# Kernel tuning notes

Measured on AMD Instinct MI355X. Metric: run time of the kernel, lower is better.

## Reference

```python
import jax, jax.numpy as jnp
import numpy as np

HID = 128
MAX_NODES = 100000
MAX_EDGES = 300000
EVT_LEN = 4096
NUM_NODE = 20000
NUM_EDGE = 320000
# EVENT_TYPE_ID_MAP: pad=0 start=1 end=2 node-add=3 node-delete=4 edge-add=5 edge-delete=6
NODE_ADD, NODE_DEL = 3, 4


def time_encode(t, time_w, time_b):
    # TimeEncoder: cos(Linear(1 -> hidden)(t))
    return jnp.cos(t[..., None] * time_w + time_b)


def gru_cell(x, h, w_ih, w_hh, b_ih, b_hh):
    gi = x @ w_ih.T + b_ih
    gh = h @ w_hh.T + b_hh
    i_r, i_z, i_n = jnp.split(gi, 3, axis=-1)
    h_r, h_z, h_n = jnp.split(gh, 3, axis=-1)
    r = jax.nn.sigmoid(i_r + h_r)
    z = jax.nn.sigmoid(i_z + h_z)
    n = jnp.tanh(i_n + r * h_n)
    return (1.0 - z) * n + z * h


def setup_inputs() -> dict:
    key = jax.random.key(0)
    ks = jax.random.split(key, 32)
    H = HID
    s = 0.05
    inp = {}
    inp["event_type_ids"] = jax.random.randint(ks[0], (EVT_LEN,), 0, 7)
    inp["src_ids"] = jax.random.randint(ks[1], (EVT_LEN,), 0, MAX_NODES)
    inp["src_mask"] = (jax.random.uniform(ks[2], (EVT_LEN,)) > 0.3).astype(jnp.float32)
    inp["dst_ids"] = jax.random.randint(ks[3], (EVT_LEN,), 0, MAX_NODES)
    inp["dst_mask"] = (jax.random.uniform(ks[4], (EVT_LEN,)) > 0.3).astype(jnp.float32)
    inp["event_edge_ids"] = jax.random.randint(ks[5], (EVT_LEN,), 0, MAX_EDGES)
    inp["event_embeddings"] = jax.random.normal(ks[6], (EVT_LEN, H), dtype=jnp.float32)
    inp["event_mask"] = (jax.random.uniform(ks[7], (EVT_LEN,)) > 0.2).astype(jnp.float32)
    inp["event_timestamps"] = jax.random.uniform(ks[8], (EVT_LEN,)) * 100.0
    inp["node_ids"] = jax.random.randint(ks[9], (NUM_NODE,), 0, MAX_NODES)
    inp["edge_ids"] = jax.random.randint(ks[10], (NUM_EDGE,), 0, MAX_EDGES)
    inp["edge_index"] = jax.random.randint(ks[11], (2, NUM_EDGE), 0, NUM_NODE)
    inp["time"] = 100
    # persistent-buffer state
    inp["memory"] = jax.random.normal(ks[12], (MAX_NODES, H), dtype=jnp.float32) * s
    inp["last_update"] = jax.random.uniform(ks[13], (MAX_EDGES,)) * 50.0
    inp["node_features"] = jax.random.normal(ks[14], (MAX_NODES, H), dtype=jnp.float32) * s
    inp["edge_features"] = jax.random.normal(ks[15], (MAX_EDGES, H), dtype=jnp.float32) * s
    # TimeEncoder params (Linear(1, H))
    inp["time_w"] = jax.random.normal(ks[16], (H,), dtype=jnp.float32) * s
    inp["time_b"] = jax.random.normal(ks[17], (H,), dtype=jnp.float32) * s
    # GRUCell(5H -> H)
    inp["gru_w_ih"] = jax.random.normal(ks[18], (3 * H, 5 * H), dtype=jnp.float32) * s
    inp["gru_w_hh"] = jax.random.normal(ks[19], (3 * H, H), dtype=jnp.float32) * s
    inp["gru_b_ih"] = jax.random.normal(ks[20], (3 * H,), dtype=jnp.float32) * s
    inp["gru_b_hh"] = jax.random.normal(ks[21], (3 * H,), dtype=jnp.float32) * s
    # TransformerConv(H, H, heads=1, edge_dim=2H)
    inp["wq"] = jax.random.normal(ks[22], (H, H), dtype=jnp.float32) * s
    inp["bq"] = jax.random.normal(ks[23], (H,), dtype=jnp.float32) * s
    inp["wk"] = jax.random.normal(ks[24], (H, H), dtype=jnp.float32) * s
    inp["bk"] = jax.random.normal(ks[25], (H,), dtype=jnp.float32) * s
    inp["wv"] = jax.random.normal(ks[26], (H, H), dtype=jnp.float32) * s
    inp["bv"] = jax.random.normal(ks[27], (H,), dtype=jnp.float32) * s
    inp["we"] = jax.random.normal(ks[28], (H, 2 * H), dtype=jnp.float32) * s  # lin_edge, no bias
    inp["wskip"] = jax.random.normal(ks[29], (H, H), dtype=jnp.float32) * s
    inp["bskip"] = jax.random.normal(ks[30], (H,), dtype=jnp.float32) * s
    return inp


def reference(event_type_ids, src_ids, src_mask, dst_ids, dst_mask, event_edge_ids,
              event_embeddings, event_mask, event_timestamps, node_ids, edge_ids,
              edge_index, time, memory, last_update, node_features, edge_features,
              time_w, time_b, gru_w_ih, gru_w_hh, gru_b_ih, gru_b_hh,
              wq, bq, wk, bk, wv, bv, we, wskip, bskip):
    H = HID
    # ---- message() ----
    L = event_type_ids.shape[0]
    type_embs = jnp.broadcast_to(event_type_ids[:, None].astype(memory.dtype), (L, H))
    src_embs = memory[src_ids] * src_mask[:, None]
    dst_embs = memory[dst_ids] * dst_mask[:, None]
    edge_last = last_update[event_edge_ids]
    rel_ts = event_timestamps - edge_last * dst_mask
    is_node_ev = ((event_type_ids == NODE_ADD) | (event_type_ids == NODE_DEL)).astype(event_timestamps.dtype)
    ts_emb = time_encode(event_timestamps * is_node_ev + rel_ts * dst_mask, time_w, time_b) * event_mask[:, None]
    src_msgs = jnp.concatenate([type_embs, src_embs, dst_embs, ts_emb, event_embeddings], axis=1) * event_mask[:, None]
    dst_msgs = jnp.concatenate([type_embs, dst_embs, src_embs, ts_emb, event_embeddings], axis=1) * dst_mask[:, None]
    # ---- agg_message(): scatter-mean over node ids ----
    def agg(msgs, ids):
        s = jax.ops.segment_sum(msgs, ids, num_segments=MAX_NODES)
        c = jax.ops.segment_sum(jnp.ones((msgs.shape[0],), msgs.dtype), ids, num_segments=MAX_NODES)
        return s / jnp.maximum(c, 1.0)[:, None]
    agg_src = agg(src_msgs, src_ids)
    agg_dst = agg(dst_msgs, dst_ids)
    # ---- GRU memory update on unique ids ----
    # torch: memory[cat(uniq_src, uniq_dst)] = rnn(...); reads use pre-update memory,
    # dst writes come after src writes so they override on overlap. Duplicate ids in
    # src_ids carry identical per-id values, so scatter-set is equivalent to unique().
    new_src = gru_cell(agg_src[src_ids], memory[src_ids], gru_w_ih, gru_w_hh, gru_b_ih, gru_b_hh)
    new_dst = gru_cell(agg_dst[dst_ids], memory[dst_ids], gru_w_ih, gru_w_hh, gru_b_ih, gru_b_hh)
    memory = memory.at[src_ids].set(new_src)
    memory = memory.at[dst_ids].set(new_dst)
    # ---- edge attributes ----
    rel_t = time - last_update[edge_ids]
    rel_t_embs = time_encode(rel_t, time_w, time_b)
    edge_attr = jnp.concatenate([rel_t_embs, edge_features[edge_ids]], axis=-1)  # (E, 2H)
    # ---- TransformerConv (heads=1, concat, root_weight) ----
    x = node_features[node_ids] + memory[node_ids]  # (N, H)
    src, dst = edge_index[0], edge_index[1]
    q = x @ wq.T + bq
    k = x @ wk.T + bk
    v = x @ wv.T + bv
    e = edge_attr @ we.T  # lin_edge (no bias)
    alpha = jnp.sum(q[dst] * (k[src] + e), axis=-1) / jnp.sqrt(jnp.asarray(H, x.dtype))
    amax = jax.ops.segment_max(alpha, dst, num_segments=x.shape[0])
    ex = jnp.exp(alpha - amax[dst])
    denom = jax.ops.segment_sum(ex, dst, num_segments=x.shape[0])
    p = ex / jnp.maximum(denom[dst], 1e-16)
    out = jax.ops.segment_sum(p[:, None] * (v[src] + e), dst, num_segments=x.shape[0])
    return out + x @ wskip.T + bskip
```

## Files before the change

kernel.cpp:

```cpp
#include <hip/hip_runtime.h>
#include <math.h>

#define HID   128
#define MAXN  100000
#define MAXE  300000
#define EVT   4096
#define NNODE 20000
#define NEDGE 320000

typedef unsigned short u16;
typedef __attribute__((ext_vector_type(8))) short bf16x8;
typedef __attribute__((ext_vector_type(4))) float f32x4;

#define OFF_WIHB      0u
#define OFF_WHHB      491520u
#define OFF_WEB       589824u
#define OFF_WALLB     655360u
#define OFF_BALL      851968u
#define BASE2         855040u
#define OFF_REP_SRC   (BASE2 + 0u)
#define OFF_REP_DST   (BASE2 + 400128u)
#define OFF_CNT_SRC   (BASE2 + 800256u)
#define OFF_CNT_DST   (BASE2 + 1200384u)
#define OFF_SUM_SRC   (BASE2 + 1600512u)
#define OFF_SUM_DST   (BASE2 + 12086272u)
#define OFF_XGB       (BASE2 + 22572032u)
#define OFF_HG        (BASE2 + 33057792u)
#define OFF_HGB       (BASE2 + 37252096u)
#define OFF_GI        (BASE2 + 39349248u)
#define OFF_GH        (BASE2 + 51932160u)
#define OFF_NEWMEM    (BASE2 + 64515072u)
#define OFF_XB        (BASE2 + 0u)
#define OFF_QKVSE     (BASE2 + 5120000u)
#define OFF_KVB       (BASE2 + 66560000u)
#define OFF_DEG       (BASE2 + 76800000u)
#define OFF_OFFS      (BASE2 + 76880128u)
#define OFF_CURSOR    (BASE2 + 76960256u)
#define OFF_BSUM      (BASE2 + 77040384u)
#define OFF_SORTED    (BASE2 + 77041664u)
#define OFF_SACCB     (BASE2 + 78321664u)

__device__ __forceinline__ float sigmoidf_(float x) { return 1.f / (1.f + __expf(-x)); }
__device__ __forceinline__ u16 f2b(float f) {
    unsigned u = __float_as_uint(f);
    unsigned r = (u + 0x7fffu + ((u >> 16) & 1u)) >> 16;
    return (u16)r;
}
__device__ __forceinline__ float b2f(unsigned h) { return __uint_as_float(h << 16); }

__global__ void k_cvt(const float* __restrict__ s, u16* __restrict__ d, int n) {
    int i = blockIdx.x * blockDim.x + threadIdx.x;
    if (i < n) d[i] = f2b(s[i]);
}

__global__ void k_tables(const int* __restrict__ src_ids, const int* __restrict__ dst_ids,
                         unsigned* rep_src, unsigned* rep_dst, int* cnt_src, int* cnt_dst) {
    int i = blockIdx.x * blockDim.x + threadIdx.x;
    if (i >= EVT) return;
    int s = src_ids[i], d = dst_ids[i];
    atomicMin(&rep_src[s], (unsigned)i);
    atomicAdd(&cnt_src[s], 1);
    atomicMin(&rep_dst[d], (unsigned)i);
    atomicAdd(&cnt_dst[d], 1);
}

__global__ void k_message(const int* __restrict__ et_ids, const int* __restrict__ src_ids,
                          const float* __restrict__ src_mask, const int* __restrict__ dst_ids,
                          const float* __restrict__ dst_mask, const int* __restrict__ ev_eids,
                          const float* __restrict__ ev_emb, const float* __restrict__ ev_mask,
                          const float* __restrict__ ev_ts, const float* __restrict__ memory,
                          const float* __restrict__ last_update, const float* __restrict__ time_w,
                          const float* __restrict__ time_b, const unsigned* __restrict__ rep_src,
                          const unsigned* __restrict__ rep_dst, const int* __restrict__ cnt_src,
                          const int* __restrict__ cnt_dst, float* sum_src, float* sum_dst) {
    int i = blockIdx.x;
    int c = threadIdx.x;
    int et = et_ids[i];
    float sm = src_mask[i], dm = dst_mask[i], em = ev_mask[i], ts = ev_ts[i];
    int sid = src_ids[i], did = dst_ids[i], eid = ev_eids[i];
    float isnode = (et == 3 || et == 4) ? 1.f : 0.f;
    float rel = ts - last_update[eid] * dm;
    float tval = ts * isnode + rel * dm;
    float tse = __cosf(tval * time_w[c] + time_b[c]) * em;
    float typ = (float)et;
    float sv = memory[(size_t)sid * HID + c] * sm;
    float dv = memory[(size_t)did * HID + c] * dm;
    float ev = ev_emb[(size_t)i * HID + c];
    float* ps = sum_src + (size_t)rep_src[sid] * 640;
    if (cnt_src[sid] == 1) {
        ps[c] = typ * em; ps[128 + c] = sv * em; ps[256 + c] = dv * em;
        ps[384 + c] = tse * em; ps[512 + c] = ev * em;
    } else {
        atomicAdd(ps + c, typ * em);
        atomicAdd(ps + 128 + c, sv * em);
        atomicAdd(ps + 256 + c, dv * em);
        atomicAdd(ps + 384 + c, tse * em);
        atomicAdd(ps + 512 + c, ev * em);
    }
    float* pd = sum_dst + (size_t)rep_dst[did] * 640;
    if (cnt_dst[did] == 1) {
        pd[c] = typ * dm; pd[128 + c] = dv * dm; pd[256 + c] = sv * dm;
        pd[384 + c] = tse * dm; pd[512 + c] = ev * dm;
    } else {
        atomicAdd(pd + c, typ * dm);
        atomicAdd(pd + 128 + c, dv * dm);
        atomicAdd(pd + 256 + c, sv * dm);
        atomicAdd(pd + 384 + c, tse * dm);
        atomicAdd(pd + 512 + c, ev * dm);
    }
}

__global__ void k_build_xg(const int* __restrict__ src_ids, const int* __restrict__ dst_ids,
                           const unsigned* __restrict__ rep_src, const unsigned* __restrict__ rep_dst,
                           const int* __restrict__ cnt_src, const int* __restrict__ cnt_dst,
                           const float* __restrict__ sum_src, const float* __restrict__ sum_dst,
                           u16* __restrict__ Xgb) {
    int r = blockIdx.x;
    int c = blockIdx.y * 128 + threadIdx.x;
    float v;
    if (r < EVT) {
        int id = src_ids[r];
        int cnt = cnt_src[id]; if (cnt < 1) cnt = 1;
        v = sum_src[(size_t)rep_src[id] * 640 + c] / (float)cnt;
    } else {
        int id = dst_ids[r - EVT];
        int cnt = cnt_dst[id]; if (cnt < 1) cnt = 1;
        v = sum_dst[(size_t)rep_dst[id] * 640 + c] / (float)cnt;
    }
    Xgb[(size_t)r * 640 + c] = f2b(v);
}

__global__ void k_build_hg(const int* __restrict__ src_ids, const int* __restrict__ dst_ids,
                           const float* __restrict__ memory, float* __restrict__ Hg,
                           u16* __restrict__ Hgb) {
    int r = blockIdx.x, c = threadIdx.x;
    int id = (r < EVT) ? src_ids[r] : dst_ids[r - EVT];
    float v = memory[(size_t)id * HID + c];
    Hg[(size_t)r * HID + c] = v;
    Hgb[(size_t)r * HID + c] = f2b(v);
}

__global__ __launch_bounds__(256) void k_gemm_mfma(const u16* __restrict__ A,
                                                   const u16* __restrict__ W,
                                                   const float* __restrict__ bias,
                                                   float* __restrict__ C,
                                                   u16* __restrict__ KVb,
                                                   int M, int N, int K, int acc) {
    __shared__ u16 Als[128 * 40];
    __shared__ u16 Wls[128 * 40];
    int tid = threadIdx.x;
    int bm = blockIdx.x * 128, bn = blockIdx.y * 128;
    int wave = tid >> 6, lane = tid & 63;
    int wm = (wave & 1) * 64, wn = (wave >> 1) * 64;
    int l15 = lane & 15, quad = lane >> 4;
    f32x4 accf[4][4] = {};
    for (int k0 = 0; k0 < K; k0 += 32) {
#pragma unroll
        for (int h = 0; h < 2; ++h) {
            int ch = tid + h * 256;
            int row = ch >> 2, kc = (ch & 3) * 8;
            int gr = bm + row;
            float4 av = make_float4(0.f, 0.f, 0.f, 0.f);
            if (gr < M) av = *(const float4*)(A + (size_t)gr * K + k0 + kc);
            *(float4*)&Als[row * 40 + kc] = av;
            int wr = bn + row;
            float4 wv_ = *(const float4*)(W + (size_t)wr * K + k0 + kc);
            *(float4*)&Wls[row * 40 + kc] = wv_;
        }
        __syncthreads();
        bf16x8 af[4], bfr[4];
#pragma unroll
        for (int r = 0; r < 4; ++r)
            af[r] = *(const bf16x8*)&Als[(wm + r * 16 + l15) * 40 + quad * 8];
#pragma unroll
        for (int c2 = 0; c2 < 4; ++c2)
            bfr[c2] = *(const bf16x8*)&Wls[(wn + c2 * 16 + l15) * 40 + quad * 8];
#pragma unroll
        for (int r = 0; r < 4; ++r)
#pragma unroll
            for (int c2 = 0; c2 < 4; ++c2)
                accf[r][c2] = __builtin_amdgcn_mfma_f32_16x16x32_bf16(af[r], bfr[c2], accf[r][c2], 0, 0, 0);
        __syncthreads();
    }
#pragma unroll
    for (int r = 0; r < 4; ++r) {
#pragma unroll
        for (int c2 = 0; c2 < 4; ++c2) {
            int ncol = bn + wn + c2 * 16 + l15;
            float bv = bias ? bias[ncol] : 0.f;
#pragma unroll
            for (int reg = 0; reg < 4; ++reg) {
                int mrow = bm + wm + r * 16 + quad * 4 + reg;
                if (mrow >= M) continue;
                float v = accf[r][c2][reg] + bv;
                if (acc) v += C[(size_t)mrow * N + ncol];
                C[(size_t)mrow * N + ncol] = v;
                if (KVb && ncol >= 128 && ncol < 384)
                    KVb[(size_t)mrow * 256 + (ncol - 128)] = f2b(v);
            }
        }
    }
}

__global__ void k_gru(const float* __restrict__ Gi, const float* __restrict__ Gh,
                      const float* __restrict__ Hg, float* __restrict__ newmem) {
    int r = blockIdx.x, c = threadIdx.x;
    const float* gi = Gi + (size_t)r * 384;
    const float* gh = Gh + (size_t)r * 384;
    float rg = sigmoidf_(gi[c] + gh[c]);
    float z  = sigmoidf_(gi[128 + c] + gh[128 + c]);
    float n  = tanhf(gi[256 + c] + rg * gh[256 + c]);
    float h  = Hg[(size_t)r * HID + c];
    newmem[(size_t)r * HID + c] = (1.f - z) * n + z * h;
}

__global__ void k_scatter(float* __restrict__ memory, const int* __restrict__ ids,
                          const float* __restrict__ newmem) {
    int i = blockIdx.x, c = threadIdx.x;
    memory[(size_t)ids[i] * HID + c] = newmem[(size_t)i * HID + c];
}

__global__ void k_wall(const float* __restrict__ wq, const float* __restrict__ wk_,
                       const float* __restrict__ wv, const float* __restrict__ wskip,
                       const float* __restrict__ we, const float* __restrict__ bq,
                       const float* __restrict__ bk, const float* __restrict__ bv,
                       const float* __restrict__ bskip, u16* __restrict__ Wallb,
                       float* __restrict__ ball) {
    int row = blockIdx.x;
    int k = threadIdx.x;
    float v;
    if (row < 128)      v = wq[row * 128 + k];
    else if (row < 256) v = wk_[(row - 128) * 128 + k];
    else if (row < 384) v = wv[(row - 256) * 128 + k];
    else if (row < 512) v = wskip[(row - 384) * 128 + k];
    else {
        int j = row - 512;
        float a = 0.f;
        for (int t = 0; t < 128; t++) a += wq[t * 128 + k] * we[t * 256 + j];
        v = a;
    }
    Wallb[row * 128 + k] = f2b(v);
    if (k == 0) {
        float b;
        if (row < 128)      b = bq[row];
        else if (row < 256) b = bk[row - 128];
        else if (row < 384) b = bv[row - 256];
        else if (row < 512) b = bskip[row - 384];
        else { int j = row - 512; float a = 0.f; for (int t = 0; t < 128; t++) a += bq[t] * we[t * 256 + j]; b = a; }
        ball[row] = b;
    }
}

__global__ void k_x(const int* __restrict__ node_ids, const float* __restrict__ nf,
                    const float* __restrict__ memory, u16* __restrict__ Xb) {
    int p = blockIdx.x, c = threadIdx.x;
    int nid = node_ids[p];
    Xb[(size_t)p * HID + c] = f2b(nf[(size_t)nid * HID + c] + memory[(size_t)nid * HID + c]);
}

__global__ void k_deg(const int* __restrict__ eidx, int* __restrict__ deg) {
    int j = blockIdx.x * blockDim.x + threadIdx.x;
    if (j >= NEDGE) return;
    atomicAdd(&deg[eidx[NEDGE + j]], 1);
}

__global__ __launch_bounds__(256) void k_scan1(const int* __restrict__ deg,
                                               int* __restrict__ offs, int* __restrict__ bsum) {
    __shared__ int wsum[4];
    int i = blockIdx.x * 256 + threadIdx.x;
    int v = (i < NNODE) ? deg[i] : 0;
    int lane = threadIdx.x & 63, w = threadIdx.x >> 6;
    int x = v;
#pragma unroll
    for (int d = 1; d < 64; d <<= 1) { int y = __shfl_up(x, d, 64); if (lane >= d) x += y; }
    if (lane == 63) wsum[w] = x;
    __syncthreads();
    int add = 0;
    for (int k = 0; k < w; ++k) add += wsum[k];
    int incl = x + add;
    if (i < NNODE) offs[i] = incl - v;
    if (threadIdx.x == 255) bsum[blockIdx.x] = incl;
}

__global__ __launch_bounds__(128) void k_scan2(int* __restrict__ bsum, int nb) {
    __shared__ int w0s;
    int t = threadIdx.x;
    int v = (t < nb) ? bsum[t] : 0;
    int lane = t & 63, w = t >> 6;
    int x = v;
#pragma unroll
    for (int d = 1; d < 64; d <<= 1) { int y = __shfl_up(x, d, 64); if (lane >= d) x += y; }
    if (t == 63) w0s = x;
    __syncthreads();
    if (w == 1) x += w0s;
    if (t < nb) bsum[t] = x - v;
}

__global__ __launch_bounds__(256) void k_scan3(int* __restrict__ offs, const int* __restrict__ bsum,
                                               int* __restrict__ cursor) {
    int i = blockIdx.x * 256 + threadIdx.x;
    if (i < NNODE) { int o = offs[i] + bsum[blockIdx.x]; offs[i] = o; cursor[i] = o; }
    if (i == 0) offs[NNODE] = NEDGE;
}

__global__ void k_sortscat(const int* __restrict__ eidx, int* __restrict__ cursor,
                           int* __restrict__ sorted) {
    int j = blockIdx.x * blockDim.x + threadIdx.x;
    if (j >= NEDGE) return;
    int d = eidx[NEDGE + j];
    int pos = atomicAdd(&cursor[d], 1);
    sorted[pos] = j;
}

__global__ __launch_bounds__(256) void k_node(const float* __restrict__ QK,
        const u16* __restrict__ KVb, const int* __restrict__ offs,
        const int* __restrict__ sorted, const int* __restrict__ eidx,
        const int* __restrict__ edge_ids, const float* __restrict__ last_update,
        const float* __restrict__ time_w, const float* __restrict__ time_b,
        const float* __restrict__ ef, const int* __restrict__ tptr,
        float* __restrict__ out, u16* __restrict__ saccb) {
    int wave = threadIdx.x >> 6, lane = threadIdx.x & 63;
    int n = blockIdx.x * 4 + wave;
    int c = 2 * lane;
    const float* base = QK + (size_t)n * 768;
    float2 qd   = *(const float2*)(base + c);
    float2 skip = *(const float2*)(base + 384 + c);
    float2 qet  = *(const float2*)(base + 512 + c);
    float2 qef  = *(const float2*)(base + 640 + c);
    float2 tw   = *(const float2*)(time_w + c);
    float2 tb   = *(const float2*)(time_b + c);
    float tf = (float)(*tptr);
    int start = offs[n], end = offs[n + 1];
    int deg = end - start;
    if (deg == 0) {
        *(float2*)(out + (size_t)n * HID + c) = skip;
        *(unsigned*)(saccb + (size_t)n * 256 + c) = 0u;
        *(unsigned*)(saccb + (size_t)n * 256 + 128 + c) = 0u;
        return;
    }
    float m = -1e30f, l_ = 0.f;
    float va0 = 0.f, va1 = 0.f, s00 = 0.f, s01 = 0.f, s10 = 0.f, s11 = 0.f;
    for (int cb = start; cb < end; cb += 64) {
        int cnt = end - cb; if (cnt > 64) cnt = 64;
        int s_l = 0, eid_l = 0; float rt_l = 0.f;
        if (lane < cnt) {
            int j = sorted[cb + lane];
            s_l = eidx[j];
            eid_l = edge_ids[j];
            rt_l = tf - last_update[eid_l];
        }
        for (int e0 = 0; e0 < cnt; e0 += 4) {
            float pv[4], cv0[4], cv1[4], vx[4], vy[4], ex[4], ey[4];
#pragma unroll
            for (int i = 0; i < 4; ++i) {
                int idx = e0 + i;
                int sel = (idx < cnt) ? idx : e0;
                int s   = __shfl(s_l, sel, 64);
                int eid = __shfl(eid_l, sel, 64);
                float rt = __shfl(rt_l, sel, 64);
                unsigned kvp = *(const unsigned*)(KVb + (size_t)s * 256 + c);
                unsigned vvp = *(const unsigned*)(KVb + (size_t)s * 256 + 128 + c);
                float2 ev = *(const float2*)(ef + (size_t)eid * HID + c);
                float k0f = b2f(kvp & 0xffffu), k1f = b2f(kvp >> 16);
                vx[i] = b2f(vvp & 0xffffu); vy[i] = b2f(vvp >> 16);
                cv0[i] = __cosf(rt * tw.x + tb.x);
                cv1[i] = __cosf(rt * tw.y + tb.y);
                ex[i] = ev.x; ey[i] = ev.y;
                pv[i] = qd.x * k0f + qd.y * k1f + qet.x * cv0[i] + qet.y * cv1[i]
                      + qef.x * ev.x + qef.y * ev.y;
            }
#pragma unroll
            for (int msk = 32; msk > 0; msk >>= 1) {
#pragma unroll
                for (int i = 0; i < 4; ++i) pv[i] += __shfl_xor(pv[i], msk, 64);
            }
            float al[4];
#pragma unroll
            for (int i = 0; i < 4; ++i)
                al[i] = (e0 + i < cnt) ? pv[i] * 0.08838834764831845f : -1e30f;
            float gm = fmaxf(fmaxf(al[0], al[1]), fmaxf(al[2], al[3]));
            if (gm > m) {
                float fac = __expf(m - gm);
                l_ *= fac; va0 *= fac; va1 *= fac;
                s00 *= fac; s01 *= fac; s10 *= fac; s11 *= fac;
                m = gm;
            }
#pragma unroll
            for (int i = 0; i < 4; ++i) {
                float w = __expf(al[i] - m);
                l_ += w;
                va0 += w * vx[i]; va1 += w * vy[i];
                s00 += w * cv0[i]; s01 += w * cv1[i];
                s10 += w * ex[i]; s11 += w * ey[i];
            }
        }
    }
    float inv = 1.f / fmaxf(l_, 1e-16f);
    float2 o; o.x = va0 * inv + skip.x; o.y = va1 * inv + skip.y;
    *(float2*)(out + (size_t)n * HID + c) = o;
    unsigned p0 = (unsigned)f2b(s00 * inv) | ((unsigned)f2b(s01 * inv) << 16);
    unsigned p1 = (unsigned)f2b(s10 * inv) | ((unsigned)f2b(s11 * inv) << 16);
    *(unsigned*)(saccb + (size_t)n * 256 + c) = p0;
    *(unsigned*)(saccb + (size_t)n * 256 + 128 + c) = p1;
}

extern "C" void kernel_launch(void* const* d_in, const int* in_sizes, int n_in,
                              void* d_out, int out_size, void* d_ws, size_t ws_size,
                              hipStream_t stream) {
    const int*   et_ids        = (const int*)d_in[0];
    const int*   src_ids       = (const int*)d_in[1];
    const float* src_mask      = (const float*)d_in[2];
    const int*   dst_ids       = (const int*)d_in[3];
    const float* dst_mask      = (const float*)d_in[4];
    const int*   ev_eids       = (const int*)d_in[5];
    const float* ev_emb        = (const float*)d_in[6];
    const float* ev_mask       = (const float*)d_in[7];
    const float* ev_ts         = (const float*)d_in[8];
    const int*   node_ids      = (const int*)d_in[9];
    const int*   edge_ids      = (const int*)d_in[10];
    const int*   edge_index    = (const int*)d_in[11];
    const int*   tptr          = (const int*)d_in[12];
    float*       memory        = (float*)d_in[13];
    const float* last_update   = (const float*)d_in[14];
    const float* node_features = (const float*)d_in[15];
    const float* edge_features = (const float*)d_in[16];
    const float* time_w        = (const float*)d_in[17];
    const float* time_b        = (const float*)d_in[18];
    const float* w_ih          = (const float*)d_in[19];
    const float* w_hh          = (const float*)d_in[20];
    const float* b_ih          = (const float*)d_in[21];
    const float* b_hh          = (const float*)d_in[22];
    const float* wq            = (const float*)d_in[23];
    const float* bq            = (const float*)d_in[24];
    const float* wk            = (const float*)d_in[25];
    const float* bk            = (const float*)d_in[26];
    const float* wv            = (const float*)d_in[27];
    const float* bv            = (const float*)d_in[28];
    const float* we            = (const float*)d_in[29];
    const float* wskip         = (const float*)d_in[30];
    const float* bskip         = (const float*)d_in[31];
    float* out = (float*)d_out;
    char*  wsb = (char*)d_ws;

    u16*   w_ih_b  = (u16*)(wsb + OFF_WIHB);
    u16*   w_hh_b  = (u16*)(wsb + OFF_WHHB);
    u16*   we_b    = (u16*)(wsb + OFF_WEB);
    u16*   Wallb   = (u16*)(wsb + OFF_WALLB);
    float* ball    = (float*)(wsb + OFF_BALL);
    unsigned* rep_src = (unsigned*)(wsb + OFF_REP_SRC);
    unsigned* rep_dst = (unsigned*)(wsb + OFF_REP_DST);
    int*   cnt_src = (int*)(wsb + OFF_CNT_SRC);
    int*   cnt_dst = (int*)(wsb + OFF_CNT_DST);
    float* sum_src = (float*)(wsb + OFF_SUM_SRC);
    float* sum_dst = (float*)(wsb + OFF_SUM_DST);
    u16*   Xgb     = (u16*)(wsb + OFF_XGB);
    float* Hg      = (float*)(wsb + OFF_HG);
    u16*   Hgb     = (u16*)(wsb + OFF_HGB);
    float* Gi      = (float*)(wsb + OFF_GI);
    float* Gh      = (float*)(wsb + OFF_GH);
    float* newmem  = (float*)(wsb + OFF_NEWMEM);
    u16*   Xb      = (u16*)(wsb + OFF_XB);
    float* QKVSE   = (float*)(wsb + OFF_QKVSE);
    u16*   KVb     = (u16*)(wsb + OFF_KVB);
    int*   deg     = (int*)(wsb + OFF_DEG);
    int*   offs    = (int*)(wsb + OFF_OFFS);
    int*   cursor  = (int*)(wsb + OFF_CURSOR);
    int*   bsum    = (int*)(wsb + OFF_BSUM);
    int*   sorted  = (int*)(wsb + OFF_SORTED);
    u16*   saccb   = (u16*)(wsb + OFF_SACCB);

    k_cvt<<<(384 * 640 + 255) / 256, 256, 0, stream>>>(w_ih, w_ih_b, 384 * 640);
    k_cvt<<<(384 * 128 + 255) / 256, 256, 0, stream>>>(w_hh, w_hh_b, 384 * 128);
    k_cvt<<<(128 * 256 + 255) / 256, 256, 0, stream>>>(we, we_b, 128 * 256);
    k_wall<<<768, 128, 0, stream>>>(wq, wk, wv, wskip, we, bq, bk, bv, bskip, Wallb, ball);

    hipMemsetAsync(wsb + OFF_REP_SRC, 0xFF, 800256, stream);
    hipMemsetAsync(wsb + OFF_CNT_SRC, 0, 800256, stream);
    hipMemsetAsync(wsb + OFF_SUM_SRC, 0, 2u * 10485760u, stream);
    k_tables<<<16, 256, 0, stream>>>(src_ids, dst_ids, rep_src, rep_dst, cnt_src, cnt_dst);
    k_message<<<EVT, 128, 0, stream>>>(et_ids, src_ids, src_mask, dst_ids, dst_mask, ev_eids,
                                       ev_emb, ev_mask, ev_ts, memory, last_update, time_w, time_b,
                                       rep_src, rep_dst, cnt_src, cnt_dst, sum_src, sum_dst);
    k_build_xg<<<dim3(2 * EVT, 5), 128, 0, stream>>>(src_ids, dst_ids, rep_src, rep_dst,
                                                     cnt_src, cnt_dst, sum_src, sum_dst, Xgb);
    k_build_hg<<<2 * EVT, 128, 0, stream>>>(src_ids, dst_ids, memory, Hg, Hgb);
    k_gemm_mfma<<<dim3(64, 3), 256, 0, stream>>>(Xgb, w_ih_b, b_ih, Gi, nullptr, 2 * EVT, 384, 640, 0);
    k_gemm_mfma<<<dim3(64, 3), 256, 0, stream>>>(Hgb, w_hh_b, b_hh, Gh, nullptr, 2 * EVT, 384, 128, 0);
    k_gru<<<2 * EVT, 128, 0, stream>>>(Gi, Gh, Hg, newmem);
    k_scatter<<<EVT, 128, 0, stream>>>(memory, src_ids, newmem);
    k_scatter<<<EVT, 128, 0, stream>>>(memory, dst_ids, newmem + (size_t)EVT * HID);

    k_x<<<NNODE, 128, 0, stream>>>(node_ids, node_features, memory, Xb);
    k_gemm_mfma<<<dim3(157, 6), 256, 0, stream>>>(Xb, Wallb, ball, QKVSE, KVb, NNODE, 768, 128, 0);
    hipMemsetAsync(wsb + OFF_DEG, 0, 80128, stream);
    k_deg<<<1250, 256, 0, stream>>>(edge_index, deg);
    k_scan1<<<79, 256, 0, stream>>>(deg, offs, bsum);
    k_scan2<<<1, 128, 0, stream>>>(bsum, 79);
    k_scan3<<<79, 256, 0, stream>>>(offs, bsum, cursor);
    k_sortscat<<<1250, 256, 0, stream>>>(edge_index, cursor, sorted);
    k_node<<<NNODE / 4, 256, 0, stream>>>(QKVSE, KVb, offs, sorted, edge_index, edge_ids,
                                          last_update, time_w, time_b, edge_features, tptr,
                                          out, saccb);
    k_gemm_mfma<<<dim3(157, 1), 256, 0, stream>>>(saccb, we_b, nullptr, out, nullptr, NNODE, 128, 256, 1);
}
```

Baseline: 557.3 us.

## Fuse small prep, zeroing, build, GEMM and scan launches to cut kernel count

Merges the weight conversion kernels and degree zeroing into one prep kernel, replaces three memsets with one zeroing kernel, and combines the table build with the degree count. It also merges the Xg/Hg build kernels, runs both GRU GEMMs in one launch, fuses the GRU with the memory scatter (skipping src rows overwritten by dst), and replaces the three-kernel scan with a single-block scan. The aim is to remove launch overhead and intermediate buffers, at the cost of a serial single-block scan. The GEMM epilogue now skips writing K/V columns to C.

```diff
diff --git a/kernel.cpp b/kernel.cpp
--- a/kernel.cpp
+++ b/kernel.cpp
@@ -48,20 +48,96 @@
 }
 __device__ __forceinline__ float b2f(unsigned h) { return __uint_as_float(h << 16); }
 
-__global__ void k_cvt(const float* __restrict__ s, u16* __restrict__ d, int n) {
-    int i = blockIdx.x * blockDim.x + threadIdx.x;
-    if (i < n) d[i] = f2b(s[i]);
-}
-
-__global__ void k_tables(const int* __restrict__ src_ids, const int* __restrict__ dst_ids,
-                         unsigned* rep_src, unsigned* rep_dst, int* cnt_src, int* cnt_dst) {
-    int i = blockIdx.x * blockDim.x + threadIdx.x;
-    if (i >= EVT) return;
-    int s = src_ids[i], d = dst_ids[i];
-    atomicMin(&rep_src[s], (unsigned)i);
-    atomicAdd(&cnt_src[s], 1);
-    atomicMin(&rep_dst[d], (unsigned)i);
-    atomicAdd(&cnt_dst[d], 1);
+__global__ void k_prep(const float* __restrict__ w_ih, const float* __restrict__ w_hh,
+                       const float* __restrict__ we,
+                       const float* __restrict__ wq, const float* __restrict__ wk_,
+                       const float* __restrict__ wv, const float* __restrict__ wskip,
+                       const float* __restrict__ bq, const float* __restrict__ bk,
+                       const float* __restrict__ bv, const float* __restrict__ bskip,
+                       u16* __restrict__ w_ih_b, u16* __restrict__ w_hh_b,
+                       u16* __restrict__ we_b, u16* __restrict__ Wallb,
+                       float* __restrict__ ball, int* __restrict__ deg) {
+    int b = blockIdx.x, t = threadIdx.x;
+    if (b < 960) {
+        int i = b * 256 + t;
+        w_ih_b[i] = f2b(w_ih[i]);
+        return;
+    }
+    b -= 960;
+    if (b < 192) {
+        int i = b * 256 + t;
+        w_hh_b[i] = f2b(w_hh[i]);
+        return;
+    }
+    b -= 192;
+    if (b < 128) {
+        int i = b * 256 + t;
+        we_b[i] = f2b(we[i]);
+        return;
+    }
+    b -= 128;
+    if (b < 79) {
+        int i = b * 256 + t;
+        if (i < NNODE) deg[i] = 0;
+        return;
+    }
+    b -= 79;
+    int idx = b * 256 + t;
+    int row = idx >> 7;
+    int k = idx & 127;
+    float v;
+    if (row < 128)      v = wq[row * 128 + k];
+    else if (row < 256) v = wk_[(row - 128) * 128 + k];
+    else if (row < 384) v = wv[(row - 256) * 128 + k];
+    else if (row < 512) v = wskip[(row - 384) * 128 + k];
+    else {
+        int j = row - 512;
+        float a = 0.f;
+        for (int t2 = 0; t2 < 128; t2++) a += wq[t2 * 128 + k] * we[t2 * 256 + j];
+        v = a;
+    }
+    Wallb[row * 128 + k] = f2b(v);
+    if (k == 0) {
+        float bb;
+        if (row < 128)      bb = bq[row];
+        else if (row < 256) bb = bk[row - 128];
+        else if (row < 384) bb = bv[row - 256];
+        else if (row < 512) bb = bskip[row - 384];
+        else { int j = row - 512; float a = 0.f; for (int t2 = 0; t2 < 128; t2++) a += bq[t2] * we[t2 * 256 + j]; bb = a; }
+        ball[row] = bb;
+    }
+}
+
+__global__ void k_zero(char* __restrict__ base) {
+    const int NFF = 50016;
+    const int NZ  = 1360736;
+    uint4 ff = make_uint4(0xFFFFFFFFu, 0xFFFFFFFFu, 0xFFFFFFFFu, 0xFFFFFFFFu);
+    uint4 zz = make_uint4(0u, 0u, 0u, 0u);
+    int idx = blockIdx.x * blockDim.x + threadIdx.x;
+    int stride = gridDim.x * blockDim.x;
+    uint4* pff = (uint4*)base;
+    uint4* pzz = (uint4*)(base + 800256);
+    for (int i = idx; i < NFF; i += stride) pff[i] = ff;
+    for (int i = idx; i < NZ; i += stride) pzz[i] = zz;
+}
+
+__global__ void k_tables_deg(const int* __restrict__ src_ids, const int* __restrict__ dst_ids,
+                             unsigned* rep_src, unsigned* rep_dst, int* cnt_src, int* cnt_dst,
+                             const int* __restrict__ eidx, int* __restrict__ deg) {
+    int b = blockIdx.x, t = threadIdx.x;
+    if (b < 16) {
+        int i = b * 256 + t;
+        if (i >= EVT) return;
+        int s = src_ids[i], d = dst_ids[i];
+        atomicMin(&rep_src[s], (unsigned)i);
+        atomicAdd(&cnt_src[s], 1);
+        atomicMin(&rep_dst[d], (unsigned)i);
+        atomicAdd(&cnt_dst[d], 1);
+    } else {
+        int j = (b - 16) * 256 + t;
+        if (j >= NEDGE) return;
+        atomicAdd(&deg[eidx[NEDGE + j]], 1);
+    }
 }
 
 __global__ void k_message(const int* __restrict__ et_ids, const int* __restrict__ src_ids,
@@ -110,13 +186,21 @@
     }
 }
 
-__global__ void k_build_xg(const int* __restrict__ src_ids, const int* __restrict__ dst_ids,
-                           const unsigned* __restrict__ rep_src, const unsigned* __restrict__ rep_dst,
-                           const int* __restrict__ cnt_src, const int* __restrict__ cnt_dst,
-                           const float* __restrict__ sum_src, const float* __restrict__ sum_dst,
-                           u16* __restrict__ Xgb) {
-    int r = blockIdx.x;
-    int c = blockIdx.y * 128 + threadIdx.x;
+__global__ void k_build(const int* __restrict__ src_ids, const int* __restrict__ dst_ids,
+                        const unsigned* __restrict__ rep_src, const unsigned* __restrict__ rep_dst,
+                        const int* __restrict__ cnt_src, const int* __restrict__ cnt_dst,
+                        const float* __restrict__ sum_src, const float* __restrict__ sum_dst,
+                        const float* __restrict__ memory, u16* __restrict__ Xgb,
+                        float* __restrict__ Hg, u16* __restrict__ Hgb) {
+    int r = blockIdx.x, y = blockIdx.y, t = threadIdx.x;
+    if (y == 5) {
+        int id = (r < EVT) ? src_ids[r] : dst_ids[r - EVT];
+        float v = memory[(size_t)id * HID + t];
+        Hg[(size_t)r * HID + t] = v;
+        Hgb[(size_t)r * HID + t] = f2b(v);
+        return;
+    }
+    int c = y * 128 + t;
     float v;
     if (r < EVT) {
         int id = src_ids[r];
@@ -130,24 +214,10 @@
     Xgb[(size_t)r * 640 + c] = f2b(v);
 }
 
-__global__ void k_build_hg(const int* __restrict__ src_ids, const int* __restrict__ dst_ids,
-                           const float* __restrict__ memory, float* __restrict__ Hg,
-                           u16* __restrict__ Hgb) {
-    int r = blockIdx.x, c = threadIdx.x;
-    int id = (r < EVT) ? src_ids[r] : dst_ids[r - EVT];
-    float v = memory[(size_t)id * HID + c];
-    Hg[(size_t)r * HID + c] = v;
-    Hgb[(size_t)r * HID + c] = f2b(v);
-}
-
-__global__ __launch_bounds__(256) void k_gemm_mfma(const u16* __restrict__ A,
-                                                   const u16* __restrict__ W,
-                                                   const float* __restrict__ bias,
-                                                   float* __restrict__ C,
-                                                   u16* __restrict__ KVb,
-                                                   int M, int N, int K, int acc) {
-    __shared__ u16 Als[128 * 40];
-    __shared__ u16 Wls[128 * 40];
+__device__ __forceinline__ void gemm_tile(const u16* __restrict__ A, const u16* __restrict__ W,
+                                          const float* __restrict__ bias, float* __restrict__ C,
+                                          u16* __restrict__ KVb, int M, int N, int K, int acc,
+                                          u16* Als, u16* Wls) {
     int tid = threadIdx.x;
     int bm = blockIdx.x * 128, bn = blockIdx.y * 128;
     int wave = tid >> 6, lane = tid & 63;
@@ -193,61 +263,56 @@
                 int mrow = bm + wm + r * 16 + quad * 4 + reg;
                 if (mrow >= M) continue;
                 float v = accf[r][c2][reg] + bv;
-                if (acc) v += C[(size_t)mrow * N + ncol];
-                C[(size_t)mrow * N + ncol] = v;
-                if (KVb && ncol >= 128 && ncol < 384)
+                if (KVb && ncol >= 128 && ncol < 384) {
                     KVb[(size_t)mrow * 256 + (ncol - 128)] = f2b(v);
+                } else {
+                    if (acc) v += C[(size_t)mrow * N + ncol];
+                    C[(size_t)mrow * N + ncol] = v;
+                }
             }
         }
     }
 }
 
-__global__ void k_gru(const float* __restrict__ Gi, const float* __restrict__ Gh,
-                      const float* __restrict__ Hg, float* __restrict__ newmem) {
+__global__ __launch_bounds__(256) void k_gemm_mfma(const u16* __restrict__ A,
+                                                   const u16* __restrict__ W,
+                                                   const float* __restrict__ bias,
+                                                   float* __restrict__ C,
+                                                   u16* __restrict__ KVb,
+                                                   int M, int N, int K, int acc) {
+    __shared__ u16 Als[128 * 40];
+    __shared__ u16 Wls[128 * 40];
+    gemm_tile(A, W, bias, C, KVb, M, N, K, acc, Als, Wls);
+}
+
+__global__ __launch_bounds__(256) void k_gemm_dual(const u16* __restrict__ A0, const u16* __restrict__ W0,
+                                                   const float* __restrict__ b0, float* __restrict__ C0,
+                                                   const u16* __restrict__ A1, const u16* __restrict__ W1,
+                                                   const float* __restrict__ b1, float* __restrict__ C1) {
+    __shared__ u16 Als[128 * 40];
+    __shared__ u16 Wls[128 * 40];
+    if (blockIdx.z == 0) gemm_tile(A0, W0, b0, C0, nullptr, 2 * EVT, 384, 640, 0, Als, Wls);
+    else                 gemm_tile(A1, W1, b1, C1, nullptr, 2 * EVT, 384, 128, 0, Als, Wls);
+}
+
+__global__ void k_gru_scatter(const float* __restrict__ Gi, const float* __restrict__ Gh,
+                              const float* __restrict__ Hg, const int* __restrict__ src_ids,
+                              const int* __restrict__ dst_ids, const unsigned* __restrict__ rep_dst,
+                              float* __restrict__ memory) {
     int r = blockIdx.x, c = threadIdx.x;
     const float* gi = Gi + (size_t)r * 384;
     const float* gh = Gh + (size_t)r * 384;
     float rg = sigmoidf_(gi[c] + gh[c]);
     float z  = sigmoidf_(gi[128 + c] + gh[128 + c]);
     float n  = tanhf(gi[256 + c] + rg * gh[256 + c]);
-    float h  = Hg[(size_t)r * HID + c];
-    newmem[(size_t)r * HID + c] = (1.f - z) * n + z * h;
-}
-
-__global__ void k_scatter(float* __restrict__ memory, const int* __restrict__ ids,
-                          const float* __restrict__ newmem) {
-    int i = blockIdx.x, c = threadIdx.x;
-    memory[(size_t)ids[i] * HID + c] = newmem[(size_t)i * HID + c];
-}
-
-__global__ void k_wall(const float* __restrict__ wq, const float* __restrict__ wk_,
-                       const float* __restrict__ wv, const float* __restrict__ wskip,
-                       const float* __restrict__ we, const float* __restrict__ bq,
-                       const float* __restrict__ bk, const float* __restrict__ bv,
-                       const float* __restrict__ bskip, u16* __restrict__ Wallb,
-                       float* __restrict__ ball) {
-    int row = blockIdx.x;
-    int k = threadIdx.x;
-    float v;
-    if (row < 128)      v = wq[row * 128 + k];
-    else if (row < 256) v = wk_[(row - 128) * 128 + k];
-    else if (row < 384) v = wv[(row - 256) * 128 + k];
-    else if (row < 512) v = wskip[(row - 384) * 128 + k];
-    else {
-        int j = row - 512;
-        float a = 0.f;
-        for (int t = 0; t < 128; t++) a += wq[t * 128 + k] * we[t * 256 + j];
-        v = a;
-    }
-    Wallb[row * 128 + k] = f2b(v);
-    if (k == 0) {
-        float b;
-        if (row < 128)      b = bq[row];
-        else if (row < 256) b = bk[row - 128];
-        else if (row < 384) b = bv[row - 256];
-        else if (row < 512) b = bskip[row - 384];
-        else { int j = row - 512; float a = 0.f; for (int t = 0; t < 128; t++) a += bq[t] * we[t * 256 + j]; b = a; }
-        ball[row] = b;
+    float h0 = Hg[(size_t)r * HID + c];
+    float h  = (1.f - z) * n + z * h0;
+    if (r < EVT) {
+        int sid = src_ids[r];
+        if (rep_dst[sid] == 0xFFFFFFFFu) memory[(size_t)sid * HID + c] = h;
+    } else {
+        int did = dst_ids[r - EVT];
+        memory[(size_t)did * HID + c] = h;
     }
 }
 
@@ -258,49 +323,26 @@
     Xb[(size_t)p * HID + c] = f2b(nf[(size_t)nid * HID + c] + memory[(size_t)nid * HID + c]);
 }
 
-__global__ void k_deg(const int* __restrict__ eidx, int* __restrict__ deg) {
-    int j = blockIdx.x * blockDim.x + threadIdx.x;
-    if (j >= NEDGE) return;
-    atomicAdd(&deg[eidx[NEDGE + j]], 1);
-}
-
-__global__ __launch_bounds__(256) void k_scan1(const int* __restrict__ deg,
-                                               int* __restrict__ offs, int* __restrict__ bsum) {
-    __shared__ int wsum[4];
-    int i = blockIdx.x * 256 + threadIdx.x;
-    int v = (i < NNODE) ? deg[i] : 0;
-    int lane = threadIdx.x & 63, w = threadIdx.x >> 6;
-    int x = v;
-#pragma unroll
-    for (int d = 1; d < 64; d <<= 1) { int y = __shfl_up(x, d, 64); if (lane >= d) x += y; }
-    if (lane == 63) wsum[w] = x;
-    __syncthreads();
-    int add = 0;
-    for (int k = 0; k < w; ++k) add += wsum[k];
-    int incl = x + add;
-    if (i < NNODE) offs[i] = incl - v;
-    if (threadIdx.x == 255) bsum[blockIdx.x] = incl;
-}
-
-__global__ __launch_bounds__(128) void k_scan2(int* __restrict__ bsum, int nb) {
-    __shared__ int w0s;
-    int t = threadIdx.x;
-    int v = (t < nb) ? bsum[t] : 0;
-    int lane = t & 63, w = t >> 6;
-    int x = v;
-#pragma unroll
-    for (int d = 1; d < 64; d <<= 1) { int y = __shfl_up(x, d, 64); if (lane >= d) x += y; }
-    if (t == 63) w0s = x;
-    __syncthreads();
-    if (w == 1) x += w0s;
-    if (t < nb) bsum[t] = x - v;
-}
-
-__global__ __launch_bounds__(256) void k_scan3(int* __restrict__ offs, const int* __restrict__ bsum,
-                                               int* __restrict__ cursor) {
-    int i = blockIdx.x * 256 + threadIdx.x;
-    if (i < NNODE) { int o = offs[i] + bsum[blockIdx.x]; offs[i] = o; cursor[i] = o; }
-    if (i == 0) offs[NNODE] = NEDGE;
+__global__ __launch_bounds__(1024) void k_scan_one(const int* __restrict__ deg,
+                                                   int* __restrict__ offs, int* __restrict__ cursor) {
+    __shared__ int wsum[16];
+    int t = threadIdx.x, lane = t & 63, w = t >> 6;
+    int carry = 0;
+    for (int base = 0; base < NNODE; base += 1024) {
+        int i = base + t;
+        int v = (i < NNODE) ? deg[i] : 0;
+        int x = v;
+#pragma unroll
+        for (int d = 1; d < 64; d <<= 1) { int y = __shfl_up(x, d, 64); if (lane >= d) x += y; }
+        if (lane == 63) wsum[w] = x;
+        __syncthreads();
+        int add = 0, tot = 0;
+        for (int k2 = 0; k2 < 16; ++k2) { int s = wsum[k2]; if (k2 < w) add += s; tot += s; }
+        if (i < NNODE) { int e = carry + add + x - v; offs[i] = e; cursor[i] = e; }
+        carry += tot;
+        __syncthreads();
+    }
+    if (t == 0) offs[NNODE] = NEDGE;
 }
 
 __global__ void k_sortscat(const int* __restrict__ eidx, int* __restrict__ cursor,
@@ -458,45 +500,33 @@
     u16*   Hgb     = (u16*)(wsb + OFF_HGB);
     float* Gi      = (float*)(wsb + OFF_GI);
     float* Gh      = (float*)(wsb + OFF_GH);
-    float* newmem  = (float*)(wsb + OFF_NEWMEM);
     u16*   Xb      = (u16*)(wsb + OFF_XB);
     float* QKVSE   = (float*)(wsb + OFF_QKVSE);
     u16*   KVb     = (u16*)(wsb + OFF_KVB);
     int*   deg     = (int*)(wsb + OFF_DEG);
     int*   offs    = (int*)(wsb + OFF_OFFS);
     int*   cursor  = (int*)(wsb + OFF_CURSOR);
-    int*   bsum    = (int*)(wsb + OFF_BSUM);
     int*   sorted  = (int*)(wsb + OFF_SORTED);
     u16*   saccb   = (u16*)(wsb + OFF_SACCB);
 
-    k_cvt<<<(384 * 640 + 255) / 256, 256, 0, stream>>>(w_ih, w_ih_b, 384 * 640);
-    k_cvt<<<(384 * 128 + 255) / 256, 256, 0, stream>>>(w_hh, w_hh_b, 384 * 128);
-    k_cvt<<<(128 * 256 + 255) / 256, 256, 0, stream>>>(we, we_b, 128 * 256);
-    k_wall<<<768, 128, 0, stream>>>(wq, wk, wv, wskip, we, bq, bk, bv, bskip, Wallb, ball);
-
-    hipMemsetAsync(wsb + OFF_REP_SRC, 0xFF, 800256, stream);
-    hipMemsetAsync(wsb + OFF_CNT_SRC, 0, 800256, stream);
-    hipMemsetAsync(wsb + OFF_SUM_SRC, 0, 2u * 10485760u, stream);
-    k_tables<<<16, 256, 0, stream>>>(src_ids, dst_ids, rep_src, rep_dst, cnt_src, cnt_dst);
+    k_prep<<<1743, 256, 0, stream>>>(w_ih, w_hh, we, wq, wk, wv, wskip, bq, bk, bv, bskip,
+                                     w_ih_b, w_hh_b, we_b, Wallb, ball, deg);
+    k_zero<<<2048, 256, 0, stream>>>(wsb + OFF_REP_SRC);
+    k_tables_deg<<<1266, 256, 0, stream>>>(src_ids, dst_ids, rep_src, rep_dst, cnt_src, cnt_dst,
+                                           edge_index, deg);
     k_message<<<EVT, 128, 0, stream>>>(et_ids, src_ids, src_mask, dst_ids, dst_mask, ev_eids,
                                        ev_emb, ev_mask, ev_ts, memory, last_update, time_w, time_b,
                                        rep_src, rep_dst, cnt_src, cnt_dst, sum_src, sum_dst);
-    k_build_xg<<<dim3(2 * EVT, 5), 128, 0, stream>>>(src_ids, dst_ids, rep_src, rep_dst,
-                                                     cnt_src, cnt_dst, sum_src, sum_dst, Xgb);
-    k_build_hg<<<2 * EVT, 128, 0, stream>>>(src_ids, dst_ids, memory, Hg, Hgb);
-    k_gemm_mfma<<<dim3(64, 3), 256, 0, stream>>>(Xgb, w_ih_b, b_ih, Gi, nullptr, 2 * EVT, 384, 640, 0);
-    k_gemm_mfma<<<dim3(64, 3), 256, 0, stream>>>(Hgb, w_hh_b, b_hh, Gh, nullptr, 2 * EVT, 384, 128, 0);
-    k_gru<<<2 * EVT, 128, 0, stream>>>(Gi, Gh, Hg, newmem);
-    k_scatter<<<EVT, 128, 0, stream>>>(memory, src_ids, newmem);
-    k_scatter<<<EVT, 128, 0, stream>>>(memory, dst_ids, newmem + (size_t)EVT * HID);
+    k_build<<<dim3(2 * EVT, 6), 128, 0, stream>>>(src_ids, dst_ids, rep_src, rep_dst,
+                                                  cnt_src, cnt_dst, sum_src, sum_dst,
+                                                  memory, Xgb, Hg, Hgb);
+    k_gemm_dual<<<dim3(64, 3, 2), 256, 0, stream>>>(Xgb, w_ih_b, b_ih, Gi,
+                                                    Hgb, w_hh_b, b_hh, Gh);
+    k_gru_scatter<<<2 * EVT, 128, 0, stream>>>(Gi, Gh, Hg, src_ids, dst_ids, rep_dst, memory);
 
     k_x<<<NNODE, 128, 0, stream>>>(node_ids, node_features, memory, Xb);
     k_gemm_mfma<<<dim3(157, 6), 256, 0, stream>>>(Xb, Wallb, ball, QKVSE, KVb, NNODE, 768, 128, 0);
-    hipMemsetAsync(wsb + OFF_DEG, 0, 80128, stream);
-    k_deg<<<1250, 256, 0, stream>>>(edge_index, deg);
-    k_scan1<<<79, 256, 0, stream>>>(deg, offs, bsum);
-    k_scan2<<<1, 128, 0, stream>>>(bsum, 79);
-    k_scan3<<<79, 256, 0, stream>>>(offs, bsum, cursor);
+    k_scan_one<<<1, 1024, 0, stream>>>(deg, offs, cursor);
     k_sortscat<<<1250, 256, 0, stream>>>(edge_index, cursor, sorted);
     k_node<<<NNODE / 4, 256, 0, stream>>>(QKVSE, KVb, offs, sorted, edge_index, edge_ids,
                                           last_update, time_w, time_b, edge_features, tptr,
```

Result: faster. 535.2 us (-4.0%).
